# Kernel tuning notes

Measured on AMD Instinct MI355X. Metric: run time of the kernel, lower is better.

Reference implementation:

```python
import jax, jax.numpy as jnp
import numpy as np

N_NODES = 100000

def _gcn_conv(x, edge_index, W, b):
    # PyG GCNConv: add self-loops, symmetric normalization, scatter-add aggregate.
    N = x.shape[0]
    loops = jnp.arange(N, dtype=edge_index.dtype)
    row = jnp.concatenate([edge_index[0], loops])  # source
    col = jnp.concatenate([edge_index[1], loops])  # target
    deg = jax.ops.segment_sum(jnp.ones_like(col, dtype=x.dtype), col, num_segments=N)
    dis = jnp.where(deg > 0, jax.lax.rsqrt(jnp.maximum(deg, 1e-12)), 0.0)
    norm = dis[row] * dis[col]                     # [E+N]
    h = x @ W                                      # [N, F_out]
    msg = norm[:, None] * h[row]                   # gather at source
    out = jax.ops.segment_sum(msg, col, num_segments=N)  # scatter-add at target
    return out + b

def setup_inputs() -> dict:
    key = jax.random.key(0)
    k = jax.random.split(key, 8)
    N, E = N_NODES, 3200000
    in_c, hid, out_c = 11, 64, 1
    x = jax.random.normal(k[0], (N, in_c), dtype=jnp.float32)
    edge_index = jax.random.randint(k[1], (2, E), 0, N, dtype=jnp.int32)
    W1 = jax.random.normal(k[2], (in_c, hid), dtype=jnp.float32) / np.sqrt(in_c)
    b1 = jnp.zeros((hid,), dtype=jnp.float32)
    W2 = jax.random.normal(k[3], (hid, hid), dtype=jnp.float32) / np.sqrt(hid)
    b2 = jnp.zeros((hid,), dtype=jnp.float32)
    Wl = jax.random.normal(k[4], (hid, out_c), dtype=jnp.float32) / np.sqrt(hid)
    bl = jnp.zeros((out_c,), dtype=jnp.float32)
    return {"x": x, "edge_index": edge_index, "W1": W1, "b1": b1,
            "W2": W2, "b2": b2, "Wl": Wl, "bl": bl}

def reference(x, edge_index, W1, b1, W2, b2, Wl, bl):
    h = jax.nn.relu(_gcn_conv(x, edge_index, W1, b1))   # dropout_p == 0 -> skipped
    h = jax.nn.relu(_gcn_conv(h, edge_index, W2, b2))
    return h @ Wl + bl
```

## Files before the change

kernel.cpp:

```cpp
#include <hip/hip_runtime.h>


#define HID 64
#define INC 11
#define XPAD 16
#define BINSH 7
#define BINW 128
#define MAXNB 800
#define ECHUNK 8192
#define SCAN_CHUNK 1024
#define STAGE_MAX 6144

typedef unsigned short bf16t;

__device__ __forceinline__ float b2f(bf16t u) {
    union { float f; unsigned int i; } v;
    v.i = ((unsigned int)u) << 16;
    return v.f;
}
__device__ __forceinline__ bf16t f2b(float f) {
    union { float ff; unsigned int i; } v;
    v.ff = f;
    unsigned int r = v.i + 0x7FFF + ((v.i >> 16) & 1);
    return (bf16t)(r >> 16);
}

__global__ void k_hist(const int* __restrict__ dst, int E, int C, int NB,
                       int* __restrict__ histT) {
    __shared__ int h[MAXNB];
    int c = blockIdx.x, t = threadIdx.x;
    for (int i = t; i < NB; i += 256) h[i] = 0;
    __syncthreads();
    int base = c * ECHUNK;
    int end = min(base + ECHUNK, E);
    int n4 = (end - base) >> 2;
    const int4* d4 = (const int4*)(dst + base);
    for (int i = t; i < n4; i += 256) {
        int4 d = d4[i];
        atomicAdd(&h[d.x >> BINSH], 1);
        atomicAdd(&h[d.y >> BINSH], 1);
        atomicAdd(&h[d.z >> BINSH], 1);
        atomicAdd(&h[d.w >> BINSH], 1);
    }
    __syncthreads();
    for (int b = t; b < NB; b += 256)
        histT[(size_t)b * C + c] = h[b];
}

__global__ void k_scan1(const int* __restrict__ in, int L,
                        int* __restrict__ part, int* __restrict__ blocksums) {
    __shared__ int lds[SCAN_CHUNK];
    __shared__ int tsum[256];
    int b = blockIdx.x, t = threadIdx.x;
    int base = b * SCAN_CHUNK;
    for (int i = t; i < SCAN_CHUNK; i += 256)
        lds[i] = (base + i < L) ? in[base + i] : 0;
    __syncthreads();
    int a0 = lds[t*4], a1 = lds[t*4+1], a2 = lds[t*4+2], a3 = lds[t*4+3];
    int ts = a0 + a1 + a2 + a3;
    tsum[t] = ts;
    __syncthreads();
    for (int off = 1; off < 256; off <<= 1) {
        int v = (t >= off) ? tsum[t - off] : 0;
        __syncthreads();
        tsum[t] += v;
        __syncthreads();
    }
    int excl = tsum[t] - ts;
    int i0 = base + t*4;
    if (i0     < L) part[i0]     = excl;
    if (i0 + 1 < L) part[i0 + 1] = excl + a0;
    if (i0 + 2 < L) part[i0 + 2] = excl + a0 + a1;
    if (i0 + 3 < L) part[i0 + 3] = excl + a0 + a1 + a2;
    if (t == 255) blocksums[b] = tsum[255];
}

__global__ void k_scan2(const int* __restrict__ blocksums, int nb, int* __restrict__ blockoff) {
    __shared__ int s[512];
    int t = threadIdx.x;
    s[t] = (t < nb) ? blocksums[t] : 0;
    __syncthreads();
    int mine = s[t];
    for (int off = 1; off < 512; off <<= 1) {
        int v = (t >= off) ? s[t - off] : 0;
        __syncthreads();
        s[t] += v;
        __syncthreads();
    }
    blockoff[t] = s[t] - mine;
}

__global__ void k_scan3f(int* __restrict__ part, const int* __restrict__ blockoff, int L) {
    int i = blockIdx.x * blockDim.x + threadIdx.x;
    if (i < L) part[i] += blockoff[i / SCAN_CHUNK];
}

__global__ void k_scatterbin(const int* __restrict__ src, const int* __restrict__ dst,
                             int E, int C, int NB, const int* __restrict__ scanT,
                             int* __restrict__ bucket) {
    __shared__ int cur[MAXNB];
    int c = blockIdx.x, t = threadIdx.x;
    for (int b = t; b < NB; b += 256) cur[b] = scanT[(size_t)b * C + c];
    __syncthreads();
    int base = c * ECHUNK;
    int end = min(base + ECHUNK, E);
    int n4 = (end - base) >> 2;
    const int4* d4 = (const int4*)(dst + base);
    const int4* s4 = (const int4*)(src + base);
    for (int i = t; i < n4; i += 512) {
        int4 da = d4[i], sa = s4[i];
        bool hb = (i + 256) < n4;
        int4 db, sb;
        if (hb) { db = d4[i + 256]; sb = s4[i + 256]; }
        int r0 = atomicAdd(&cur[da.x >> BINSH], 1);
        int r1 = atomicAdd(&cur[da.y >> BINSH], 1);
        int r2 = atomicAdd(&cur[da.z >> BINSH], 1);
        int r3 = atomicAdd(&cur[da.w >> BINSH], 1);
        int r4 = 0, r5 = 0, r6 = 0, r7 = 0;
        if (hb) {
            r4 = atomicAdd(&cur[db.x >> BINSH], 1);
            r5 = atomicAdd(&cur[db.y >> BINSH], 1);
            r6 = atomicAdd(&cur[db.z >> BINSH], 1);
            r7 = atomicAdd(&cur[db.w >> BINSH], 1);
        }
        bucket[r0] = (sa.x << BINSH) | (da.x & (BINW - 1));
        bucket[r1] = (sa.y << BINSH) | (da.y & (BINW - 1));
        bucket[r2] = (sa.z << BINSH) | (da.z & (BINW - 1));
        bucket[r3] = (sa.w << BINSH) | (da.w & (BINW - 1));
        if (hb) {
            bucket[r4] = (sb.x << BINSH) | (db.x & (BINW - 1));
            bucket[r5] = (sb.y << BINSH) | (db.y & (BINW - 1));
            bucket[r6] = (sb.z << BINSH) | (db.z & (BINW - 1));
            bucket[r7] = (sb.w << BINSH) | (db.w & (BINW - 1));
        }
    }
}

__global__ void k_csrbuild(const int* __restrict__ scanT, int C, int NB, int E,
                           const int* __restrict__ bucket, int* __restrict__ csr,
                           int* __restrict__ rowptr, float* __restrict__ dis, int N) {
    __shared__ int cnt[BINW];
    __shared__ int ex[BINW];
    __shared__ int cur[BINW];
    __shared__ int stage[STAGE_MAX];
    int b = blockIdx.x, t = threadIdx.x;
    int s = scanT[(size_t)b * C];
    int e = (b + 1 < NB) ? scanT[(size_t)(b + 1) * C] : E;
    int len = e - s;
    if (t < BINW) cnt[t] = 0;
    __syncthreads();
    for (int p = s + t; p < e; p += 256)
        atomicAdd(&cnt[bucket[p] & (BINW - 1)], 1);
    __syncthreads();
    if (t < BINW) ex[t] = cnt[t];
    __syncthreads();
    for (int off = 1; off < BINW; off <<= 1) {
        int v = (t < BINW && t >= off) ? ex[t - off] : 0;
        __syncthreads();
        if (t < BINW) ex[t] += v;
        __syncthreads();
    }
    if (t < BINW) {
        int excl = ex[t] - cnt[t];
        cur[t] = excl;
        int n = b * BINW + t;
        if (n <= N) rowptr[n] = s + excl;
        if (n < N)  dis[n] = rsqrtf((float)(cnt[t] + 1));
    }
    __syncthreads();
    if (len <= STAGE_MAX) {
        for (int p = s + t; p < e; p += 256) {
            int w = bucket[p];
            int r = atomicAdd(&cur[w & (BINW - 1)], 1);
            stage[r] = w >> BINSH;
        }
        __syncthreads();
        for (int i = t; i < len; i += 256) csr[s + i] = stage[i];
    } else {
        for (int p = s + t; p < e; p += 256) {
            int w = bucket[p];
            int r = atomicAdd(&cur[w & (BINW - 1)], 1);
            csr[s + r] = w >> BINSH;
        }
    }
}

__global__ void k_xs(const float* __restrict__ x, const float* __restrict__ dis,
                     bf16t* __restrict__ xs, int N) {
    int i = blockIdx.x * blockDim.x + threadIdx.x;
    if (i < N * XPAD) {
        int row = i >> 4, f = i & 15;
        float v = (f < INC) ? dis[row] * x[row * INC + f] : 0.f;
        xs[i] = f2b(v);
    }
}

__global__ void k_agg1x(const int* __restrict__ rowptr, const int* __restrict__ csr,
                        const bf16t* __restrict__ xs, const float* __restrict__ dis,
                        const float* __restrict__ W1, const float* __restrict__ b1,
                        const float* __restrict__ W2, bf16t* __restrict__ g2, int N) {
    __shared__ float W1s[INC * HID];
    __shared__ float W2s[HID * HID];
    __shared__ float arow[4][HID];
    int t = threadIdx.x;
    for (int i = t; i < INC * HID; i += 256) W1s[i] = W1[i];
    for (int i = t; i < HID * HID; i += 256) W2s[i] = W2[i];
    __syncthreads();
    int lane = t & 63, wv = t >> 6;
    int row = (blockIdx.x * blockDim.x + t) >> 6;
    if (row >= N) return;
    int f = lane & 15, e = lane >> 4;
    int p0 = rowptr[row], p1 = rowptr[row + 1];
    float acc = 0.f;
    for (int p = p0; p < p1; p += 64) {
        int idx = (p + lane < p1) ? csr[p + lane] : 0;
        int ng = min(64, p1 - p);
        int j = 0;
        for (; j + 8 <= ng; j += 8) {
            int sa = __shfl(idx, j + e);
            int sb = __shfl(idx, j + 4 + e);
            bf16t ua = xs[(size_t)sa * XPAD + f];
            bf16t ub = xs[(size_t)sb * XPAD + f];
            acc += b2f(ua); acc += b2f(ub);
        }
        for (; j < ng; j += 4) {
            int q = j + e;
            int s_ = __shfl(idx, (q < ng) ? q : 0);
            bf16t u = xs[(size_t)s_ * XPAD + f];
            acc += (q < ng) ? b2f(u) : 0.f;
        }
    }
    acc += __shfl_xor(acc, 32);
    acc += __shfl_xor(acc, 16);
    acc += b2f(xs[(size_t)row * XPAD + f]);
    float d = dis[row];
    float pre = 0.f;
    #pragma unroll
    for (int k = 0; k < INC; ++k)
        pre += __shfl(acc, k) * W1s[k * HID + lane];
    float a = d * pre + b1[lane];
    a = a > 0.f ? a : 0.f;
    arow[wv][lane] = a;
    float acc2 = 0.f;
    #pragma unroll
    for (int k = 0; k < HID; k += 4) {
        float a0 = arow[wv][k], a1 = arow[wv][k+1], a2 = arow[wv][k+2], a3 = arow[wv][k+3];
        acc2 += a0 * W2s[(k    ) * HID + lane];
        acc2 += a1 * W2s[(k + 1) * HID + lane];
        acc2 += a2 * W2s[(k + 2) * HID + lane];
        acc2 += a3 * W2s[(k + 3) * HID + lane];
    }
    g2[(size_t)row * HID + lane] = f2b(d * acc2);
}

__device__ __forceinline__ float agg_row_b(const int* __restrict__ rowptr,
                                           const int* __restrict__ csr,
                                           const bf16t* __restrict__ g,
                                           int row, int lane) {
    int s = rowptr[row], e = rowptr[row + 1];
    float acc = b2f(g[(size_t)row * HID + lane]);
    for (int p = s; p < e; p += 64) {
        int idx = (p + lane < e) ? csr[p + lane] : 0;
        int cnt = min(64, e - p);
        int j = 0;
        for (; j + 7 < cnt; j += 8) {
            int s0 = __shfl(idx, j);
            int s1 = __shfl(idx, j + 1);
            int s2 = __shfl(idx, j + 2);
            int s3 = __shfl(idx, j + 3);
            int s4 = __shfl(idx, j + 4);
            int s5 = __shfl(idx, j + 5);
            int s6 = __shfl(idx, j + 6);
            int s7 = __shfl(idx, j + 7);
            bf16t v0 = g[(size_t)s0 * HID + lane];
            bf16t v1 = g[(size_t)s1 * HID + lane];
            bf16t v2 = g[(size_t)s2 * HID + lane];
            bf16t v3 = g[(size_t)s3 * HID + lane];
            bf16t v4 = g[(size_t)s4 * HID + lane];
            bf16t v5 = g[(size_t)s5 * HID + lane];
            bf16t v6 = g[(size_t)s6 * HID + lane];
            bf16t v7 = g[(size_t)s7 * HID + lane];
            acc += b2f(v0); acc += b2f(v1); acc += b2f(v2); acc += b2f(v3);
            acc += b2f(v4); acc += b2f(v5); acc += b2f(v6); acc += b2f(v7);
        }
        for (; j < cnt; ++j)
            acc += b2f(g[(size_t)__shfl(idx, j) * HID + lane]);
    }
    return acc;
}

__global__ void k_agg2_head(const int* __restrict__ rowptr, const int* __restrict__ csr,
                            const bf16t* __restrict__ g, const float* __restrict__ dis,
                            const float* __restrict__ b, const float* __restrict__ Wl,
                            const float* __restrict__ bl, float* __restrict__ out, int N) {
    int lane = threadIdx.x & 63;
    int row = (blockIdx.x * blockDim.x + threadIdx.x) >> 6;
    if (row >= N) return;
    float acc = agg_row_b(rowptr, csr, g, row, lane);
    float v = dis[row] * acc + b[lane];
    v = v > 0.f ? v : 0.f;
    v *= Wl[lane];
    #pragma unroll
    for (int off = 32; off > 0; off >>= 1) v += __shfl_down(v, off);
    if (lane == 0) out[row] = v + bl[0];
}

extern "C" void kernel_launch(void* const* d_in, const int* in_sizes, int n_in,
                              void* d_out, int out_size, void* d_ws, size_t ws_size,
                              hipStream_t stream) {
    const float* x  = (const float*)d_in[0];
    const int*   ei = (const int*)d_in[1];
    const float* W1 = (const float*)d_in[2];
    const float* b1 = (const float*)d_in[3];
    const float* W2 = (const float*)d_in[4];
    const float* b2 = (const float*)d_in[5];
    const float* Wl = (const float*)d_in[6];
    const float* bl = (const float*)d_in[7];
    float* out = (float*)d_out;

    const int N = in_sizes[0] / INC;
    const int E = in_sizes[1] / 2;
    const int NB = (N + BINW - 1) / BINW;
    const int C  = (E + ECHUNK - 1) / ECHUNK;
    const int L  = NB * C;
    const int nScan = (L + SCAN_CHUNK - 1) / SCAN_CHUNK;

    char* ws = (char*)d_ws;
    size_t off = 0;
    auto alloc = [&](size_t bytes) { void* p = ws + off; off += (bytes + 255) / 256 * 256; return p; };
    int*   histT    = (int*)alloc((size_t)L * 4);
    int*   blocksums= (int*)alloc(512 * 4);
    int*   blockoff = (int*)alloc(512 * 4);
    int*   rowptr   = (int*)alloc((size_t)(N + 1) * 4);
    float* dis      = (float*)alloc((size_t)N * 4);
    int*   csr      = (int*)alloc((size_t)E * 4);
    int*   bucket   = (int*)alloc((size_t)E * 4);
    bf16t* xs       = (bf16t*)alloc((size_t)N * XPAD * 2);
    bf16t* g2       = (bf16t*)alloc((size_t)N * HID * 2);

    const int TPB = 256;
    const int* esrc = ei;
    const int* edst = ei + E;
    const int waveBlocks = ((size_t)N * 64 + TPB - 1) / TPB;

    k_hist<<<C, TPB, 0, stream>>>(edst, E, C, NB, histT);
    k_scan1<<<nScan, TPB, 0, stream>>>(histT, L, histT, blocksums);
    k_scan2<<<1, 512, 0, stream>>>(blocksums, nScan, blockoff);
    k_scan3f<<<(L + TPB - 1) / TPB, TPB, 0, stream>>>(histT, blockoff, L);
    k_scatterbin<<<C, TPB, 0, stream>>>(esrc, edst, E, C, NB, histT, bucket);
    k_csrbuild<<<NB, TPB, 0, stream>>>(histT, C, NB, E, bucket, csr, rowptr, dis, N);

    k_xs<<<((N * XPAD) + TPB - 1) / TPB, TPB, 0, stream>>>(x, dis, xs, N);

    k_agg1x<<<waveBlocks, TPB, 0, stream>>>(rowptr, csr, xs, dis, W1, b1, W2, g2, N);

    k_agg2_head<<<waveBlocks, TPB, 0, stream>>>(rowptr, csr, g2, dis, b2, Wl, bl, out, N);
}
```

Baseline: 229.3 us.

## Vectorize neighbor gathers with 8 edges per wave step in both aggregation kernels

Both aggregation kernels now have each wave process 8 neighbors at once. Each lane loads a wide chunk of the source row (a 16-byte uint4 of 8 bf16 values in layer 2, a 4-byte pair in layer 1), and the partial sums are reduced with xor shuffles across lane groups. This replaces per-lane 2-byte loads that touched one neighbor row per step, cutting load instruction count and raising memory-level parallelism. The layer-2 matvec in agg1 now reads a padded, transposed W2 from shared memory with float4 reads. This costs more registers and adds reduction shuffles at the end of each row.

```diff
diff --git a/kernel.cpp b/kernel.cpp
--- a/kernel.cpp
+++ b/kernel.cpp
@@ -23,6 +23,12 @@
     v.ff = f;
     unsigned int r = v.i + 0x7FFF + ((v.i >> 16) & 1);
     return (bf16t)(r >> 16);
+}
+__device__ __forceinline__ float blo(unsigned int u) {
+    union { float f; unsigned int i; } v; v.i = u << 16; return v.f;
+}
+__device__ __forceinline__ float bhi(unsigned int u) {
+    union { float f; unsigned int i; } v; v.i = u & 0xFFFF0000u; return v.f;
 }
 
 __global__ void k_hist(const int* __restrict__ dst, int E, int C, int NB,
@@ -200,109 +206,121 @@
                         const float* __restrict__ W1, const float* __restrict__ b1,
                         const float* __restrict__ W2, bf16t* __restrict__ g2, int N) {
     __shared__ float W1s[INC * HID];
-    __shared__ float W2s[HID * HID];
-    __shared__ float arow[4][HID];
+    __shared__ __align__(16) float W2Ts[HID][HID + 4];
+    __shared__ __align__(16) float arow[4][HID];
     int t = threadIdx.x;
     for (int i = t; i < INC * HID; i += 256) W1s[i] = W1[i];
-    for (int i = t; i < HID * HID; i += 256) W2s[i] = W2[i];
+    for (int i = t; i < HID * HID; i += 256) W2Ts[i & 63][i >> 6] = W2[i];
     __syncthreads();
     int lane = t & 63, wv = t >> 6;
     int row = (blockIdx.x * blockDim.x + t) >> 6;
     if (row >= N) return;
-    int f = lane & 15, e = lane >> 4;
+    int pr = lane & 7;
+    int slot = lane >> 3;
     int p0 = rowptr[row], p1 = rowptr[row + 1];
-    float acc = 0.f;
+    float a0 = 0.f, a1 = 0.f;
     for (int p = p0; p < p1; p += 64) {
         int idx = (p + lane < p1) ? csr[p + lane] : 0;
-        int ng = min(64, p1 - p);
-        int j = 0;
-        for (; j + 8 <= ng; j += 8) {
-            int sa = __shfl(idx, j + e);
-            int sb = __shfl(idx, j + 4 + e);
-            bf16t ua = xs[(size_t)sa * XPAD + f];
-            bf16t ub = xs[(size_t)sb * XPAD + f];
-            acc += b2f(ua); acc += b2f(ub);
-        }
-        for (; j < ng; j += 4) {
-            int q = j + e;
-            int s_ = __shfl(idx, (q < ng) ? q : 0);
-            bf16t u = xs[(size_t)s_ * XPAD + f];
-            acc += (q < ng) ? b2f(u) : 0.f;
-        }
-    }
-    acc += __shfl_xor(acc, 32);
-    acc += __shfl_xor(acc, 16);
-    acc += b2f(xs[(size_t)row * XPAD + f]);
+        int cnt = min(64, p1 - p);
+        for (int j = 0; j * 8 < cnt; ++j) {
+            int q = j * 8 + slot;
+            int srcn = __shfl(idx, q);
+            unsigned int u = *(const unsigned int*)(xs + (size_t)srcn * XPAD + pr * 2);
+            float m = (q < cnt) ? 1.f : 0.f;
+            a0 = fmaf(m, blo(u), a0);
+            a1 = fmaf(m, bhi(u), a1);
+        }
+    }
+    #pragma unroll
+    for (int mask = 8; mask <= 32; mask <<= 1) {
+        a0 += __shfl_xor(a0, mask);
+        a1 += __shfl_xor(a1, mask);
+    }
+    {
+        unsigned int us = *(const unsigned int*)(xs + (size_t)row * XPAD + pr * 2);
+        a0 += blo(us);
+        a1 += bhi(us);
+    }
     float d = dis[row];
     float pre = 0.f;
     #pragma unroll
-    for (int k = 0; k < INC; ++k)
-        pre += __shfl(acc, k) * W1s[k * HID + lane];
+    for (int k = 0; k < INC; ++k) {
+        float xv = (k & 1) ? __shfl(a1, k >> 1) : __shfl(a0, k >> 1);
+        pre += xv * W1s[k * HID + lane];
+    }
     float a = d * pre + b1[lane];
     a = a > 0.f ? a : 0.f;
     arow[wv][lane] = a;
+    const float4* ar4 = (const float4*)&arow[wv][0];
+    const float4* wr4 = (const float4*)&W2Ts[lane][0];
     float acc2 = 0.f;
     #pragma unroll
-    for (int k = 0; k < HID; k += 4) {
-        float a0 = arow[wv][k], a1 = arow[wv][k+1], a2 = arow[wv][k+2], a3 = arow[wv][k+3];
-        acc2 += a0 * W2s[(k    ) * HID + lane];
-        acc2 += a1 * W2s[(k + 1) * HID + lane];
-        acc2 += a2 * W2s[(k + 2) * HID + lane];
-        acc2 += a3 * W2s[(k + 3) * HID + lane];
+    for (int k4 = 0; k4 < 16; ++k4) {
+        float4 av = ar4[k4];
+        float4 wv4 = wr4[k4];
+        acc2 += av.x * wv4.x + av.y * wv4.y + av.z * wv4.z + av.w * wv4.w;
     }
     g2[(size_t)row * HID + lane] = f2b(d * acc2);
-}
-
-__device__ __forceinline__ float agg_row_b(const int* __restrict__ rowptr,
-                                           const int* __restrict__ csr,
-                                           const bf16t* __restrict__ g,
-                                           int row, int lane) {
-    int s = rowptr[row], e = rowptr[row + 1];
-    float acc = b2f(g[(size_t)row * HID + lane]);
-    for (int p = s; p < e; p += 64) {
-        int idx = (p + lane < e) ? csr[p + lane] : 0;
-        int cnt = min(64, e - p);
-        int j = 0;
-        for (; j + 7 < cnt; j += 8) {
-            int s0 = __shfl(idx, j);
-            int s1 = __shfl(idx, j + 1);
-            int s2 = __shfl(idx, j + 2);
-            int s3 = __shfl(idx, j + 3);
-            int s4 = __shfl(idx, j + 4);
-            int s5 = __shfl(idx, j + 5);
-            int s6 = __shfl(idx, j + 6);
-            int s7 = __shfl(idx, j + 7);
-            bf16t v0 = g[(size_t)s0 * HID + lane];
-            bf16t v1 = g[(size_t)s1 * HID + lane];
-            bf16t v2 = g[(size_t)s2 * HID + lane];
-            bf16t v3 = g[(size_t)s3 * HID + lane];
-            bf16t v4 = g[(size_t)s4 * HID + lane];
-            bf16t v5 = g[(size_t)s5 * HID + lane];
-            bf16t v6 = g[(size_t)s6 * HID + lane];
-            bf16t v7 = g[(size_t)s7 * HID + lane];
-            acc += b2f(v0); acc += b2f(v1); acc += b2f(v2); acc += b2f(v3);
-            acc += b2f(v4); acc += b2f(v5); acc += b2f(v6); acc += b2f(v7);
-        }
-        for (; j < cnt; ++j)
-            acc += b2f(g[(size_t)__shfl(idx, j) * HID + lane]);
-    }
-    return acc;
 }
 
 __global__ void k_agg2_head(const int* __restrict__ rowptr, const int* __restrict__ csr,
                             const bf16t* __restrict__ g, const float* __restrict__ dis,
-                            const float* __restrict__ b, const float* __restrict__ Wl,
+                            const float* __restrict__ b2, const float* __restrict__ Wl,
                             const float* __restrict__ bl, float* __restrict__ out, int N) {
     int lane = threadIdx.x & 63;
     int row = (blockIdx.x * blockDim.x + threadIdx.x) >> 6;
     if (row >= N) return;
-    float acc = agg_row_b(rowptr, csr, g, row, lane);
-    float v = dis[row] * acc + b[lane];
-    v = v > 0.f ? v : 0.f;
-    v *= Wl[lane];
+    int h = lane & 7;
+    int slot = lane >> 3;
+    int s = rowptr[row], e = rowptr[row + 1];
+    float a0 = 0.f, a1 = 0.f, a2 = 0.f, a3 = 0.f, a4 = 0.f, a5 = 0.f, a6 = 0.f, a7 = 0.f;
+    for (int p = s; p < e; p += 64) {
+        int idx = (p + lane < e) ? csr[p + lane] : 0;
+        int cnt = min(64, e - p);
+        for (int j = 0; j * 8 < cnt; ++j) {
+            int q = j * 8 + slot;
+            int srcn = __shfl(idx, q);
+            const uint4 gv = *(const uint4*)(g + (size_t)srcn * HID + h * 8);
+            float m = (q < cnt) ? 1.f : 0.f;
+            a0 = fmaf(m, blo(gv.x), a0); a1 = fmaf(m, bhi(gv.x), a1);
+            a2 = fmaf(m, blo(gv.y), a2); a3 = fmaf(m, bhi(gv.y), a3);
+            a4 = fmaf(m, blo(gv.z), a4); a5 = fmaf(m, bhi(gv.z), a5);
+            a6 = fmaf(m, blo(gv.w), a6); a7 = fmaf(m, bhi(gv.w), a7);
+        }
+    }
     #pragma unroll
-    for (int off = 32; off > 0; off >>= 1) v += __shfl_down(v, off);
-    if (lane == 0) out[row] = v + bl[0];
+    for (int mask = 8; mask <= 32; mask <<= 1) {
+        a0 += __shfl_xor(a0, mask); a1 += __shfl_xor(a1, mask);
+        a2 += __shfl_xor(a2, mask); a3 += __shfl_xor(a3, mask);
+        a4 += __shfl_xor(a4, mask); a5 += __shfl_xor(a5, mask);
+        a6 += __shfl_xor(a6, mask); a7 += __shfl_xor(a7, mask);
+    }
+    {
+        const uint4 gv = *(const uint4*)(g + (size_t)row * HID + h * 8);
+        a0 += blo(gv.x); a1 += bhi(gv.x);
+        a2 += blo(gv.y); a3 += bhi(gv.y);
+        a4 += blo(gv.z); a5 += bhi(gv.z);
+        a6 += blo(gv.w); a7 += bhi(gv.w);
+    }
+    float d = dis[row];
+    float4 blo4 = *(const float4*)(b2 + h * 8);
+    float4 bhi4 = *(const float4*)(b2 + h * 8 + 4);
+    float4 wlo4 = *(const float4*)(Wl + h * 8);
+    float4 whi4 = *(const float4*)(Wl + h * 8 + 4);
+    float part = 0.f;
+    float v;
+    v = d * a0 + blo4.x; v = v > 0.f ? v : 0.f; part += v * wlo4.x;
+    v = d * a1 + blo4.y; v = v > 0.f ? v : 0.f; part += v * wlo4.y;
+    v = d * a2 + blo4.z; v = v > 0.f ? v : 0.f; part += v * wlo4.z;
+    v = d * a3 + blo4.w; v = v > 0.f ? v : 0.f; part += v * wlo4.w;
+    v = d * a4 + bhi4.x; v = v > 0.f ? v : 0.f; part += v * whi4.x;
+    v = d * a5 + bhi4.y; v = v > 0.f ? v : 0.f; part += v * whi4.y;
+    v = d * a6 + bhi4.z; v = v > 0.f ? v : 0.f; part += v * whi4.z;
+    v = d * a7 + bhi4.w; v = v > 0.f ? v : 0.f; part += v * whi4.w;
+    part += __shfl_xor(part, 1);
+    part += __shfl_xor(part, 2);
+    part += __shfl_xor(part, 4);
+    if (lane == 0) out[row] = part + bl[0];
 }
 
 extern "C" void kernel_launch(void* const* d_in, const int* in_sizes, int n_in,
```

Result: faster. 216.4 us (-5.6%).
